# Kernel tuning notes

Measured on AMD Instinct MI355X. Metric: run time of the kernel, lower is better.

## Reference

```python
import jax, jax.numpy as jnp
import numpy as np

NEG_SLOPE = 0.2  # LeakyReLU slope used by GAT attention
EPS = 1e-16


def gat_conv(x, edge_index, W, a_src, a_dst, b):
    """One GATConv layer with 'mean' head aggregation.
    x: [N, Fin], edge_index: [2, E] (row 0 = src/j, row 1 = dst/i),
    W: [Fin, H*F], a_src/a_dst: [H, F], b: [F].
    Returns [N, F].
    """
    N = x.shape[0]
    H, F = a_src.shape
    h = (x @ W).reshape(N, H, F)                      # [N, H, F]
    src, dst = edge_index[0], edge_index[1]
    # per-node attention halves, gathered per edge
    as_ = jnp.einsum('nhf,hf->nh', h, a_src)          # [N, H]
    ad_ = jnp.einsum('nhf,hf->nh', h, a_dst)          # [N, H]
    e = jax.nn.leaky_relu(as_[src] + ad_[dst], NEG_SLOPE)  # [E, H]
    # segment softmax over incoming edges of each dst node
    m = jax.ops.segment_max(e, dst, num_segments=N)   # [N, H]
    ex = jnp.exp(e - m[dst])                          # [E, H]
    denom = jax.ops.segment_sum(ex, dst, num_segments=N)
    alpha = ex / (denom[dst] + EPS)                   # [E, H]
    # weighted scatter-aggregate of source features
    out = jax.ops.segment_sum(alpha[:, :, None] * h[src], dst, num_segments=N)  # [N, H, F]
    return out.mean(axis=1) + b                       # mean over heads


def setup_inputs() -> dict:
    key = jax.random.key(0)
    ks = jax.random.split(key, 10)
    N, E = 100000, 1000000
    in_dim, hid, out_dim, H = 128, 32, 16, 4
    x = jax.random.normal(ks[0], (N, in_dim), dtype=jnp.float32)
    edge_index = jax.random.randint(ks[1], (2, E), 0, N, dtype=jnp.int64)
    s1 = 1.0 / np.sqrt(in_dim)
    s2 = 1.0 / np.sqrt(hid)
    W1 = jax.random.uniform(ks[2], (in_dim, H * hid), jnp.float32, -s1, s1)
    a1_src = jax.random.uniform(ks[3], (H, hid), jnp.float32, -s2, s2)
    a1_dst = jax.random.uniform(ks[4], (H, hid), jnp.float32, -s2, s2)
    b1 = jnp.zeros((hid,), jnp.float32)
    s3 = 1.0 / np.sqrt(out_dim)
    W2 = jax.random.uniform(ks[5], (hid, H * out_dim), jnp.float32, -s2, s2)
    a2_src = jax.random.uniform(ks[6], (H, out_dim), jnp.float32, -s3, s3)
    a2_dst = jax.random.uniform(ks[7], (H, out_dim), jnp.float32, -s3, s3)
    b2 = jnp.zeros((out_dim,), jnp.float32)
    return {"x": x, "edge_index": edge_index,
            "W1": W1, "a1_src": a1_src, "a1_dst": a1_dst, "b1": b1,
            "W2": W2, "a2_src": a2_src, "a2_dst": a2_dst, "b2": b2}


def reference(x, edge_index, W1, a1_src, a1_dst, b1, W2, a2_src, a2_dst, b2):
    h = gat_conv(x, edge_index, W1, a1_src, a1_dst, b1)
    h = jax.nn.relu(h)
    # dropout is identity in eval mode
    out = gat_conv(h, edge_index, W2, a2_src, a2_dst, b2)
    return out
```

## Files before the change

kernel.cpp:

```cpp
#include <hip/hip_runtime.h>
#include <math.h>

#define NEG_SLOPE 0.2f
#define EPS_GAT 1e-16f
typedef unsigned int u32;
typedef unsigned short u16;
typedef __attribute__((ext_vector_type(8))) short short8;
typedef __attribute__((ext_vector_type(4))) float f32x4;

__device__ inline u16 f2bf(float x) {
    union { float f; u32 u; } v; v.f = x;
    u32 r = v.u + 0x7FFFu + ((v.u >> 16) & 1u);
    return (u16)(r >> 16);
}
__device__ inline float bf_lo(u32 u) {
    union { u32 i; float f; } v; v.i = u << 16; return v.f;
}
__device__ inline float bf_hi(u32 u) {
    union { u32 i; float f; } v; v.i = u & 0xFFFF0000u; return v.f;
}
__device__ inline float bf1(u16 s) {
    union { u32 i; float f; } v; v.i = ((u32)s) << 16; return v.f;
}
__device__ inline float lrelu_exp(float e) {
    e = fmaxf(e, NEG_SLOPE * e);
    return __expf(e);
}


__global__ void degree_kernel(const int* __restrict__ dst, int E,
                              int* __restrict__ counts, int* __restrict__ rank) {
    int e = blockIdx.x * blockDim.x + threadIdx.x;
    if (e < E) rank[e] = atomicAdd(&counts[dst[e]], 1);
}

__global__ __launch_bounds__(1024) void scan_block_kernel(const int* __restrict__ counts, int N,
                                                          int* __restrict__ scanned, int* __restrict__ bsums) {
    __shared__ int tmp[1024];
    int i = blockIdx.x * 1024 + threadIdx.x;
    int v = (i < N) ? counts[i] : 0;
    tmp[threadIdx.x] = v;
    __syncthreads();
    for (int d = 1; d < 1024; d <<= 1) {
        int t = (threadIdx.x >= d) ? tmp[threadIdx.x - d] : 0;
        __syncthreads();
        tmp[threadIdx.x] += t;
        __syncthreads();
    }
    if (i < N) scanned[i] = tmp[threadIdx.x];
    if (threadIdx.x == 1023) bsums[blockIdx.x] = tmp[1023];
}

__global__ __launch_bounds__(256) void scan_partials_kernel(int* __restrict__ bsums, int nb) {
    __shared__ int tmp[256];
    int tid = threadIdx.x;
    int v = (tid < nb) ? bsums[tid] : 0;
    tmp[tid] = v;
    __syncthreads();
    for (int d = 1; d < 256; d <<= 1) {
        int t = (tid >= d) ? tmp[tid - d] : 0;
        __syncthreads();
        tmp[tid] += t;
        __syncthreads();
    }
    if (tid < nb) bsums[tid] = tmp[tid] - v;
}

__global__ void finalize_offsets_kernel(const int* __restrict__ scanned,
                                        const int* __restrict__ bsums_excl, int N,
                                        int* __restrict__ row_off) {
    int i = blockIdx.x * blockDim.x + threadIdx.x;
    if (i < N) {
        int incl = scanned[i] + bsums_excl[i >> 10];
        row_off[i + 1] = incl;
        if (i == 0) row_off[0] = 0;
    }
}

__global__ void fill_csr_kernel(const int* __restrict__ src, const int* __restrict__ dst, int E,
                                const int* __restrict__ row_off, const int* __restrict__ rank,
                                int* __restrict__ csr_src) {
    int e = blockIdx.x * blockDim.x + threadIdx.x;
    if (e < E) {
        int pos = row_off[dst[e]] + rank[e];
        csr_src[pos] = src[e];
    }
}


__global__ void conv_w1t_kernel(const float* __restrict__ W1,
                                u16* __restrict__ w1t_hi, u16* __restrict__ w1t_lo) {
    int i = blockIdx.x * blockDim.x + threadIdx.x;
    int k = i >> 7, n = i & 127;
    float w = W1[i];
    u16 hi = f2bf(w);
    u16 lo = f2bf(w - bf1(hi));
    w1t_hi[n * 128 + k] = hi;
    w1t_lo[n * 128 + k] = lo;
}


__global__ __launch_bounds__(256) void gemm1_mfma_kernel(const float* __restrict__ X,
                                                         const u16* __restrict__ w1t_hi,
                                                         const u16* __restrict__ w1t_lo,
                                                         u16* __restrict__ Hb, int N) {
    __shared__ u16 xsh_hi[64][40];
    __shared__ u16 xsh_lo[64][40];
    __shared__ u16 wsh_hi[128][40];
    __shared__ u16 wsh_lo[128][40];
    int tid = threadIdx.x;
    int wave = tid >> 6, lane = tid & 63, quad = lane >> 4;
    int m0 = blockIdx.x * 64;

    f32x4 acc[4][2];
#pragma unroll
    for (int rt = 0; rt < 4; ++rt)
#pragma unroll
        for (int ct = 0; ct < 2; ++ct) acc[rt][ct] = (f32x4)(0.f);

    int xrow = tid >> 2, xkq = (tid & 3) * 8;

    for (int k0 = 0; k0 < 128; k0 += 32) {
        {
            int gr = m0 + xrow;
            float f[8];
            *(float4*)&f[0] = (gr < N) ? *(const float4*)(X + (size_t)gr * 128 + k0 + xkq)
                                       : make_float4(0.f, 0.f, 0.f, 0.f);
            *(float4*)&f[4] = (gr < N) ? *(const float4*)(X + (size_t)gr * 128 + k0 + xkq + 4)
                                       : make_float4(0.f, 0.f, 0.f, 0.f);
            u16 hi[8], lo[8];
#pragma unroll
            for (int i = 0; i < 8; ++i) {
                hi[i] = f2bf(f[i]);
                lo[i] = f2bf(f[i] - bf1(hi[i]));
            }
            *(uint4*)&xsh_hi[xrow][xkq] = *(uint4*)hi;
            *(uint4*)&xsh_lo[xrow][xkq] = *(uint4*)lo;
        }
        {
#pragma unroll
            for (int i = 0; i < 2; ++i) {
                int id = tid * 2 + i;
                int n = id >> 2, part = id & 3;
                *(uint4*)&wsh_hi[n][part * 8] =
                    ((const uint4*)(w1t_hi + n * 128 + k0))[part];
                *(uint4*)&wsh_lo[n][part * 8] =
                    ((const uint4*)(w1t_lo + n * 128 + k0))[part];
            }
        }
        __syncthreads();

        short8 bhi[2], blo[2];
#pragma unroll
        for (int ct = 0; ct < 2; ++ct) {
            int n = wave * 32 + ct * 16 + (lane & 15);
            bhi[ct] = *(const short8*)&wsh_hi[n][quad * 8];
            blo[ct] = *(const short8*)&wsh_lo[n][quad * 8];
        }
#pragma unroll
        for (int rt = 0; rt < 4; ++rt) {
            int m = rt * 16 + (lane & 15);
            short8 ahi = *(const short8*)&xsh_hi[m][quad * 8];
            short8 alo = *(const short8*)&xsh_lo[m][quad * 8];
#pragma unroll
            for (int ct = 0; ct < 2; ++ct) {
                acc[rt][ct] = __builtin_amdgcn_mfma_f32_16x16x32_bf16(ahi, bhi[ct], acc[rt][ct], 0, 0, 0);
                acc[rt][ct] = __builtin_amdgcn_mfma_f32_16x16x32_bf16(alo, bhi[ct], acc[rt][ct], 0, 0, 0);
                acc[rt][ct] = __builtin_amdgcn_mfma_f32_16x16x32_bf16(ahi, blo[ct], acc[rt][ct], 0, 0, 0);
            }
        }
        __syncthreads();
    }

#pragma unroll
    for (int rt = 0; rt < 4; ++rt)
#pragma unroll
        for (int ct = 0; ct < 2; ++ct) {
            int col = wave * 32 + ct * 16 + (lane & 15);
#pragma unroll
            for (int r = 0; r < 4; ++r) {
                int gr = m0 + rt * 16 + quad * 4 + r;
                if (gr < N) Hb[(size_t)gr * 128 + col] = f2bf(acc[rt][ct][r]);
            }
        }
}


__global__ void attn1_kernel(const u16* __restrict__ Hb, const float* __restrict__ a_src,
                             const float* __restrict__ a_dst, float* __restrict__ as_,
                             float* __restrict__ ad_, int N) {
    int t = blockIdx.x * blockDim.x + threadIdx.x;
    int n = t >> 2, h = t & 3;
    if (n >= N) return;
    const u32* hr = (const u32*)(Hb + (size_t)n * 128 + h * 32);
    const float* av = a_src + h * 32;
    const float* bv = a_dst + h * 32;
    float s1 = 0.f, s2 = 0.f;
#pragma unroll
    for (int q = 0; q < 4; ++q) {
        uint4 u = *(const uint4*)(hr + q * 4);
        float f0 = bf_lo(u.x), f1 = bf_hi(u.x);
        float f2 = bf_lo(u.y), f3 = bf_hi(u.y);
        float f4 = bf_lo(u.z), f5 = bf_hi(u.z);
        float f6 = bf_lo(u.w), f7 = bf_hi(u.w);
        int k = q * 8;
        s1 += f0 * av[k] + f1 * av[k + 1] + f2 * av[k + 2] + f3 * av[k + 3]
            + f4 * av[k + 4] + f5 * av[k + 5] + f6 * av[k + 6] + f7 * av[k + 7];
        s2 += f0 * bv[k] + f1 * bv[k + 1] + f2 * bv[k + 2] + f3 * bv[k + 3]
            + f4 * bv[k + 4] + f5 * bv[k + 5] + f6 * bv[k + 6] + f7 * bv[k + 7];
    }
    as_[n * 4 + h] = s1;
    ad_[n * 4 + h] = s2;
}


__global__ __launch_bounds__(256) void node_agg128_kernel(const u32* __restrict__ Hb,
                                                          const float* __restrict__ as_,
                                                          const float* __restrict__ ad_,
                                                          const int* __restrict__ row_off,
                                                          const int* __restrict__ csr_src,
                                                          const float* __restrict__ bias,
                                                          u32* __restrict__ O1, int N) {
    int lane = threadIdx.x & 63;
    int node = __builtin_amdgcn_readfirstlane(blockIdx.x * 4 + (threadIdx.x >> 6));
    if (node >= N) return;
    int start = __builtin_amdgcn_readfirstlane(row_off[node]);
    int end   = __builtin_amdgcn_readfirstlane(row_off[node + 1]);
    int h = lane >> 4;
    float adh = ad_[node * 4 + h];

    float ax = 0.f, ay = 0.f, den = 0.f;
    int j = start;
    for (; j + 4 <= end; j += 4) {
        int s0 = __builtin_amdgcn_readfirstlane(csr_src[j]);
        int s1 = __builtin_amdgcn_readfirstlane(csr_src[j + 1]);
        int s2 = __builtin_amdgcn_readfirstlane(csr_src[j + 2]);
        int s3 = __builtin_amdgcn_readfirstlane(csr_src[j + 3]);
        float a0 = as_[s0 * 4 + h], a1 = as_[s1 * 4 + h];
        float a2 = as_[s2 * 4 + h], a3 = as_[s3 * 4 + h];
        u32 u0 = Hb[s0 * 64 + lane];
        u32 u1 = Hb[s1 * 64 + lane];
        u32 u2 = Hb[s2 * 64 + lane];
        u32 u3 = Hb[s3 * 64 + lane];
        float e0 = lrelu_exp(a0 + adh), e1 = lrelu_exp(a1 + adh);
        float e2 = lrelu_exp(a2 + adh), e3 = lrelu_exp(a3 + adh);
        ax += e0 * bf_lo(u0); ay += e0 * bf_hi(u0); den += e0;
        ax += e1 * bf_lo(u1); ay += e1 * bf_hi(u1); den += e1;
        ax += e2 * bf_lo(u2); ay += e2 * bf_hi(u2); den += e2;
        ax += e3 * bf_lo(u3); ay += e3 * bf_hi(u3); den += e3;
    }
    for (; j < end; ++j) {
        int s = __builtin_amdgcn_readfirstlane(csr_src[j]);
        float e = lrelu_exp(as_[s * 4 + h] + adh);
        u32 u = Hb[s * 64 + lane];
        ax += e * bf_lo(u); ay += e * bf_hi(u); den += e;
    }
    float inv = 1.f / (den + EPS_GAT);
    float px = ax * inv, py = ay * inv;
    px += __shfl_xor(px, 16); py += __shfl_xor(py, 16);
    px += __shfl_xor(px, 32); py += __shfl_xor(py, 32);
    if (lane < 16) {
        int f = lane * 2;
        float ox = fmaxf(px * 0.25f + bias[f], 0.f);
        float oy = fmaxf(py * 0.25f + bias[f + 1], 0.f);
        O1[node * 16 + lane] = (u32)f2bf(ox) | ((u32)f2bf(oy) << 16);
    }
}


__global__ void fold_w2_kernel(const float* __restrict__ W2, const float* __restrict__ a2s,
                               const float* __restrict__ a2d, float* __restrict__ w_as,
                               float* __restrict__ w_ad) {
    int t = threadIdx.x;
    int h = t >> 5, k = t & 31;
    float s1 = 0.f, s2 = 0.f;
#pragma unroll
    for (int f = 0; f < 16; ++f) {
        float w = W2[k * 64 + h * 16 + f];
        s1 += w * a2s[h * 16 + f];
        s2 += w * a2d[h * 16 + f];
    }
    w_as[h * 32 + k] = s1;
    w_ad[h * 32 + k] = s2;
}

__global__ void attn2_kernel(const u32* __restrict__ O1, const float* __restrict__ w_as,
                             const float* __restrict__ w_ad, float* __restrict__ as_,
                             float* __restrict__ ad_, int N) {
    int t = blockIdx.x * blockDim.x + threadIdx.x;
    int n = t >> 2, h = t & 3;
    if (n >= N) return;
    const u32* r = O1 + (size_t)n * 16;
    const float* wa = w_as + h * 32;
    const float* wd = w_ad + h * 32;
    float s1 = 0.f, s2 = 0.f;
#pragma unroll
    for (int q = 0; q < 4; ++q) {
        uint4 u = *(const uint4*)(r + q * 4);
        float f0 = bf_lo(u.x), f1 = bf_hi(u.x);
        float f2 = bf_lo(u.y), f3 = bf_hi(u.y);
        float f4 = bf_lo(u.z), f5 = bf_hi(u.z);
        float f6 = bf_lo(u.w), f7 = bf_hi(u.w);
        int k = q * 8;
        s1 += f0 * wa[k] + f1 * wa[k + 1] + f2 * wa[k + 2] + f3 * wa[k + 3]
            + f4 * wa[k + 4] + f5 * wa[k + 5] + f6 * wa[k + 6] + f7 * wa[k + 7];
        s2 += f0 * wd[k] + f1 * wd[k + 1] + f2 * wd[k + 2] + f3 * wd[k + 3]
            + f4 * wd[k + 4] + f5 * wd[k + 5] + f6 * wd[k + 6] + f7 * wd[k + 7];
    }
    as_[n * 4 + h] = s1;
    ad_[n * 4 + h] = s2;
}


__global__ __launch_bounds__(256) void node_agg32_fused_kernel(const u32* __restrict__ O1,
                                                               const float* __restrict__ as_,
                                                               const float* __restrict__ ad_,
                                                               const int* __restrict__ row_off,
                                                               const int* __restrict__ csr_src,
                                                               const float* __restrict__ W2,
                                                               const float* __restrict__ b2,
                                                               float* __restrict__ Out, int N) {
    __shared__ float w2sh[2048];
    __shared__ float aggsh[4][128];
    int tid = threadIdx.x;
    {
        float4 v = ((const float4*)W2)[tid];
        *(float4*)&w2sh[tid * 4] = v;
        float4 v2 = ((const float4*)W2)[tid + 256];
        *(float4*)&w2sh[(tid + 256) * 4] = v2;
    }
    __syncthreads();

    int lane = tid & 63;
    int nb = tid >> 6;
    int node = __builtin_amdgcn_readfirstlane(blockIdx.x * 4 + nb);
    bool active = node < N;
    if (active) {
        int start = __builtin_amdgcn_readfirstlane(row_off[node]);
        int end   = __builtin_amdgcn_readfirstlane(row_off[node + 1]);
        int h = lane >> 4, f = lane & 15;
        float adh = ad_[node * 4 + h];

        float ax = 0.f, ay = 0.f, den = 0.f;
        int j = start;
        for (; j + 4 <= end; j += 4) {
            int s0 = __builtin_amdgcn_readfirstlane(csr_src[j]);
            int s1 = __builtin_amdgcn_readfirstlane(csr_src[j + 1]);
            int s2 = __builtin_amdgcn_readfirstlane(csr_src[j + 2]);
            int s3 = __builtin_amdgcn_readfirstlane(csr_src[j + 3]);
            float a0 = as_[s0 * 4 + h], a1 = as_[s1 * 4 + h];
            float a2 = as_[s2 * 4 + h], a3 = as_[s3 * 4 + h];
            u32 u0 = O1[s0 * 16 + f];
            u32 u1 = O1[s1 * 16 + f];
            u32 u2 = O1[s2 * 16 + f];
            u32 u3 = O1[s3 * 16 + f];
            float e0 = lrelu_exp(a0 + adh), e1 = lrelu_exp(a1 + adh);
            float e2 = lrelu_exp(a2 + adh), e3 = lrelu_exp(a3 + adh);
            ax += e0 * bf_lo(u0); ay += e0 * bf_hi(u0); den += e0;
            ax += e1 * bf_lo(u1); ay += e1 * bf_hi(u1); den += e1;
            ax += e2 * bf_lo(u2); ay += e2 * bf_hi(u2); den += e2;
            ax += e3 * bf_lo(u3); ay += e3 * bf_hi(u3); den += e3;
        }
        for (; j < end; ++j) {
            int s = __builtin_amdgcn_readfirstlane(csr_src[j]);
            float e = lrelu_exp(as_[s * 4 + h] + adh);
            u32 u = O1[s * 16 + f];
            ax += e * bf_lo(u); ay += e * bf_hi(u); den += e;
        }
        float inv = 1.f / (den + EPS_GAT);
        aggsh[nb][h * 32 + f * 2]     = ax * inv;
        aggsh[nb][h * 32 + f * 2 + 1] = ay * inv;
    }
    __syncthreads();

    if (tid < 64) {
        int nb2 = tid >> 4, o = tid & 15;
        int node2 = blockIdx.x * 4 + nb2;
        if (node2 < N) {
            float s = 0.f;
#pragma unroll
            for (int h = 0; h < 4; ++h) {
                const float* a = &aggsh[nb2][h * 32];
                const float* w = &w2sh[h * 16 + o];
#pragma unroll
                for (int k = 0; k < 32; ++k)
                    s += a[k] * w[k * 64];
            }
            Out[(size_t)node2 * 16 + o] = s * 0.25f + b2[o];
        }
    }
}


extern "C" void kernel_launch(void* const* d_in, const int* in_sizes, int n_in,
                              void* d_out, int out_size, void* d_ws, size_t ws_size,
                              hipStream_t stream) {
    const float* x      = (const float*)d_in[0];
    const int*   eidx   = (const int*)d_in[1];
    const float* W1     = (const float*)d_in[2];
    const float* a1_src = (const float*)d_in[3];
    const float* a1_dst = (const float*)d_in[4];
    const float* b1     = (const float*)d_in[5];
    const float* W2     = (const float*)d_in[6];
    const float* a2_src = (const float*)d_in[7];
    const float* a2_dst = (const float*)d_in[8];
    const float* b2     = (const float*)d_in[9];
    float* out = (float*)d_out;

    const int N = in_sizes[0] / 128;
    const int E = in_sizes[1] / 2;
    const int* src = eidx;
    const int* dst = eidx + E;

    char* base = (char*)d_ws;
    size_t off = 0;
    auto carve = [&](size_t bytes) -> char* {
        off = (off + 255) & ~(size_t)255;
        char* p = base + off;
        off += bytes;
        return p;
    };
    int* counts   = (int*)carve((size_t)N * 4);
    int* scanned  = (int*)carve((size_t)N * 4);
    int* bsums    = (int*)carve(256 * 4);
    int* row_off  = (int*)carve((size_t)(N + 1) * 4);
    int* rank     = (int*)carve((size_t)E * 4);
    int* csr_src  = (int*)carve((size_t)E * 4);
    u16* w1t_hi   = (u16*)carve(128 * 128 * 2);
    u16* w1t_lo   = (u16*)carve(128 * 128 * 2);
    u16* h1b      = (u16*)carve((size_t)N * 128 * 2);
    u32* out1b    = (u32*)carve((size_t)N * 16 * 4);
    float* as1  = (float*)carve((size_t)N * 4 * 4);
    float* ad1  = (float*)carve((size_t)N * 4 * 4);
    float* as2  = (float*)carve((size_t)N * 4 * 4);
    float* ad2  = (float*)carve((size_t)N * 4 * 4);
    float* w_as = (float*)carve(4 * 32 * 4);
    float* w_ad = (float*)carve(4 * 32 * 4);
    (void)ws_size; (void)n_in; (void)out_size;

    hipMemsetAsync(counts, 0, (size_t)N * 4, stream);
    degree_kernel<<<(E + 255) / 256, 256, 0, stream>>>(dst, E, counts, rank);
    int nb = (N + 1023) / 1024;
    scan_block_kernel<<<nb, 1024, 0, stream>>>(counts, N, scanned, bsums);
    scan_partials_kernel<<<1, 256, 0, stream>>>(bsums, nb);
    finalize_offsets_kernel<<<(N + 255) / 256, 256, 0, stream>>>(scanned, bsums, N, row_off);
    fill_csr_kernel<<<(E + 255) / 256, 256, 0, stream>>>(src, dst, E, row_off, rank, csr_src);

    conv_w1t_kernel<<<64, 256, 0, stream>>>(W1, w1t_hi, w1t_lo);
    gemm1_mfma_kernel<<<(N + 63) / 64, 256, 0, stream>>>(x, w1t_hi, w1t_lo, h1b, N);
    attn1_kernel<<<(N * 4 + 255) / 256, 256, 0, stream>>>(h1b, a1_src, a1_dst, as1, ad1, N);
    node_agg128_kernel<<<(N + 3) / 4, 256, 0, stream>>>((const u32*)h1b, as1, ad1,
                                                        row_off, csr_src, b1, out1b, N);

    fold_w2_kernel<<<1, 128, 0, stream>>>(W2, a2_src, a2_dst, w_as, w_ad);
    attn2_kernel<<<(N * 4 + 255) / 256, 256, 0, stream>>>(out1b, w_as, w_ad, as2, ad2, N);
    node_agg32_fused_kernel<<<(N + 3) / 4, 256, 0, stream>>>(out1b, as2, ad2, row_off,
                                                             csr_src, W2, b2, out, N);
}
```

Before: 347.8 us.

## Preload neighbor indices per wave and parallelize fused W2 projection across lanes

Both aggregation kernels now load up to 64 neighbor indices with one coalesced vector load and broadcast them with lane shuffles, replacing serial scalar loads of csr_src. Edges past the first 64 fall back to the old scalar-load loop. The layer-2 fused kernel also spreads the final 128x16 projection over all 256 threads, with one head per 16-lane group reduced by xor shuffles, instead of 64 threads each doing 128 MACs. It pads the shared aggregation buffer and drops the first barrier. That barrier removal looks like a race, since the W2 shared-memory fill is now only ordered by the later __syncthreads, which still precedes the reads.

```diff
diff --git a/kernel.cpp b/kernel.cpp
--- a/kernel.cpp
+++ b/kernel.cpp
@@ -226,16 +226,21 @@
     if (node >= N) return;
     int start = __builtin_amdgcn_readfirstlane(row_off[node]);
     int end   = __builtin_amdgcn_readfirstlane(row_off[node + 1]);
+    int deg = end - start;
     int h = lane >> 4;
     float adh = ad_[node * 4 + h];
 
+    int clamp = (deg > 0) ? deg - 1 : 0;
+    int vidx = csr_src[start + min(lane, clamp)];
+    int m = min(deg, 64);
+
     float ax = 0.f, ay = 0.f, den = 0.f;
-    int j = start;
-    for (; j + 4 <= end; j += 4) {
-        int s0 = __builtin_amdgcn_readfirstlane(csr_src[j]);
-        int s1 = __builtin_amdgcn_readfirstlane(csr_src[j + 1]);
-        int s2 = __builtin_amdgcn_readfirstlane(csr_src[j + 2]);
-        int s3 = __builtin_amdgcn_readfirstlane(csr_src[j + 3]);
+    int j = 0;
+    for (; j + 4 <= m; j += 4) {
+        int s0 = __shfl(vidx, j);
+        int s1 = __shfl(vidx, j + 1);
+        int s2 = __shfl(vidx, j + 2);
+        int s3 = __shfl(vidx, j + 3);
         float a0 = as_[s0 * 4 + h], a1 = as_[s1 * 4 + h];
         float a2 = as_[s2 * 4 + h], a3 = as_[s3 * 4 + h];
         u32 u0 = Hb[s0 * 64 + lane];
@@ -249,8 +254,14 @@
         ax += e2 * bf_lo(u2); ay += e2 * bf_hi(u2); den += e2;
         ax += e3 * bf_lo(u3); ay += e3 * bf_hi(u3); den += e3;
     }
-    for (; j < end; ++j) {
-        int s = __builtin_amdgcn_readfirstlane(csr_src[j]);
+    for (; j < m; ++j) {
+        int s = __shfl(vidx, j);
+        float e = lrelu_exp(as_[s * 4 + h] + adh);
+        u32 u = Hb[s * 64 + lane];
+        ax += e * bf_lo(u); ay += e * bf_hi(u); den += e;
+    }
+    for (int jj = start + 64; jj < end; ++jj) {
+        int s = __builtin_amdgcn_readfirstlane(csr_src[jj]);
         float e = lrelu_exp(as_[s * 4 + h] + adh);
         u32 u = Hb[s * 64 + lane];
         ax += e * bf_lo(u); ay += e * bf_hi(u); den += e;
@@ -321,7 +332,7 @@
                                                                const float* __restrict__ b2,
                                                                float* __restrict__ Out, int N) {
     __shared__ float w2sh[2048];
-    __shared__ float aggsh[4][128];
+    __shared__ float aggsh[4][136];
     int tid = threadIdx.x;
     {
         float4 v = ((const float4*)W2)[tid];
@@ -329,25 +340,29 @@
         float4 v2 = ((const float4*)W2)[tid + 256];
         *(float4*)&w2sh[(tid + 256) * 4] = v2;
     }
-    __syncthreads();
 
     int lane = tid & 63;
     int nb = tid >> 6;
     int node = __builtin_amdgcn_readfirstlane(blockIdx.x * 4 + nb);
     bool active = node < N;
+    int h = lane >> 4, f = lane & 15;
     if (active) {
         int start = __builtin_amdgcn_readfirstlane(row_off[node]);
         int end   = __builtin_amdgcn_readfirstlane(row_off[node + 1]);
-        int h = lane >> 4, f = lane & 15;
+        int deg = end - start;
         float adh = ad_[node * 4 + h];
 
+        int clamp = (deg > 0) ? deg - 1 : 0;
+        int vidx = csr_src[start + min(lane, clamp)];
+        int m = min(deg, 64);
+
         float ax = 0.f, ay = 0.f, den = 0.f;
-        int j = start;
-        for (; j + 4 <= end; j += 4) {
-            int s0 = __builtin_amdgcn_readfirstlane(csr_src[j]);
-            int s1 = __builtin_amdgcn_readfirstlane(csr_src[j + 1]);
-            int s2 = __builtin_amdgcn_readfirstlane(csr_src[j + 2]);
-            int s3 = __builtin_amdgcn_readfirstlane(csr_src[j + 3]);
+        int j = 0;
+        for (; j + 4 <= m; j += 4) {
+            int s0 = __shfl(vidx, j);
+            int s1 = __shfl(vidx, j + 1);
+            int s2 = __shfl(vidx, j + 2);
+            int s3 = __shfl(vidx, j + 3);
             float a0 = as_[s0 * 4 + h], a1 = as_[s1 * 4 + h];
             float a2 = as_[s2 * 4 + h], a3 = as_[s3 * 4 + h];
             u32 u0 = O1[s0 * 16 + f];
@@ -361,33 +376,34 @@
             ax += e2 * bf_lo(u2); ay += e2 * bf_hi(u2); den += e2;
             ax += e3 * bf_lo(u3); ay += e3 * bf_hi(u3); den += e3;
         }
-        for (; j < end; ++j) {
-            int s = __builtin_amdgcn_readfirstlane(csr_src[j]);
+        for (; j < m; ++j) {
+            int s = __shfl(vidx, j);
             float e = lrelu_exp(as_[s * 4 + h] + adh);
             u32 u = O1[s * 16 + f];
             ax += e * bf_lo(u); ay += e * bf_hi(u); den += e;
         }
+        for (int jj = start + 64; jj < end; ++jj) {
+            int s = __builtin_amdgcn_readfirstlane(csr_src[jj]);
+            float e = lrelu_exp(as_[s * 4 + h] + adh);
+            u32 u = O1[s * 16 + f];
+            ax += e * bf_lo(u); ay += e * bf_hi(u); den += e;
+        }
         float inv = 1.f / (den + EPS_GAT);
-        aggsh[nb][h * 32 + f * 2]     = ax * inv;
-        aggsh[nb][h * 32 + f * 2 + 1] = ay * inv;
+        aggsh[nb][h * 34 + f * 2]     = ax * inv;
+        aggsh[nb][h * 34 + f * 2 + 1] = ay * inv;
     }
     __syncthreads();
 
-    if (tid < 64) {
-        int nb2 = tid >> 4, o = tid & 15;
-        int node2 = blockIdx.x * 4 + nb2;
-        if (node2 < N) {
-            float s = 0.f;
-#pragma unroll
-            for (int h = 0; h < 4; ++h) {
-                const float* a = &aggsh[nb2][h * 32];
-                const float* w = &w2sh[h * 16 + o];
-#pragma unroll
-                for (int k = 0; k < 32; ++k)
-                    s += a[k] * w[k * 64];
-            }
-            Out[(size_t)node2 * 16 + o] = s * 0.25f + b2[o];
-        }
+    if (active) {
+        int q = h, o = f;
+        float s = 0.f;
+#pragma unroll
+        for (int k = 0; k < 32; ++k)
+            s += aggsh[nb][q * 34 + k] * w2sh[k * 64 + q * 16 + o];
+        s += __shfl_xor(s, 16);
+        s += __shfl_xor(s, 32);
+        if (lane < 16)
+            Out[(size_t)node * 16 + o] = s * 0.25f + b2[o];
     }
 }
 
```

Result: faster. 329.5 us (-5.3%).
